# Performance work log

Measured on AMD Instinct MI355X. Metric: run time of the kernel, lower is better.

Reference implementation:

```python
import jax, jax.numpy as jnp
import numpy as np

B, T, D, H = 8, 256, 1024, 512
NUM_SPANS = T * (T + 1) // 2          # triangular span enumeration
K = int(2.0 * T)                      # pruning_ratio * num_tokens
NUM_GOLD = 10
NEG = -1e20                           # allennlp replace_masked_values fill

# static triangular (start, end) index tables: for start in range(T): for end in range(start, T)
_starts = np.repeat(np.arange(T), np.arange(T, 0, -1))
_ends = np.concatenate([np.arange(s, T) for s in range(T)])
START_IDX = jnp.asarray(_starts, dtype=jnp.int32)
END_IDX = jnp.asarray(_ends, dtype=jnp.int32)


def setup_inputs() -> dict:
    key = jax.random.key(0)
    ks = jax.random.split(key, 8)
    inputs = jax.random.normal(ks[0], (B, T, D), dtype=jnp.float32)
    input_mask = jnp.ones((B, T), dtype=jnp.int32)
    # gold spans with start <= end, all in range (sorted along last dim)
    answer_spans = jnp.sort(jax.random.randint(ks[1], (B, NUM_GOLD, 2), 0, T), axis=-1)
    sD = 1.0 / np.sqrt(D)
    sH = 1.0 / np.sqrt(H)
    W_start = jax.random.uniform(ks[2], (D, H), jnp.float32, -sD, sD)
    b_start = jax.random.uniform(ks[3], (H,), jnp.float32, -sD, sD)
    W_end = jax.random.uniform(ks[4], (D, H), jnp.float32, -sD, sD)
    b_end = jax.random.uniform(ks[5], (H,), jnp.float32, -sD, sD)
    w_score = jax.random.uniform(ks[6], (H, 1), jnp.float32, -sH, sH)
    b_score = jax.random.uniform(ks[7], (1,), jnp.float32, -sH, sH)
    return {"inputs": inputs, "input_mask": input_mask, "answer_spans": answer_spans,
            "W_start": W_start, "b_start": b_start, "W_end": W_end, "b_end": b_end,
            "w_score": w_score, "b_score": b_score}


def reference(inputs, input_mask, answer_spans, W_start, b_start, W_end, b_end, w_score, b_score):
    # SpanRepAssembly: project starts/ends, pairwise-sum over triangular spans
    hs = inputs @ W_start + b_start                        # [B,T,H]
    he = inputs @ W_end + b_end                            # [B,T,H]
    span_hidden = hs[:, START_IDX, :] + he[:, END_IDX, :]  # [B,S,H]
    m = input_mask.astype(bool)
    span_mask = m[:, START_IDX] & m[:, END_IDX]            # [B,S]

    # span scorer: ReLU -> Linear(H,1)
    scores = jax.nn.relu(span_hidden) @ w_score + b_score  # [B,S,1]
    scores = jnp.where(span_mask[..., None], scores, NEG)

    # Pruner: top-k by score, indices sorted ascending, gather
    _, top_idx = jax.lax.top_k(scores[..., 0], K)          # [B,K]
    top_idx = jnp.sort(top_idx, axis=1)
    top_logits = jnp.take_along_axis(scores, top_idx[..., None], axis=1)       # [B,K,1]
    top_mask = jnp.take_along_axis(span_mask, top_idx, axis=1)[..., None].astype(jnp.float32)
    top_probs = jax.nn.sigmoid(top_logits) * top_mask

    # gold prediction map (union policy): labels[b, tri_index(span)] = 1
    s0 = answer_spans[..., 0].astype(jnp.int32)
    e0 = answer_spans[..., 1].astype(jnp.int32)
    gmask = (s0 >= 0)
    arg_idx = (2 * s0 * T - s0 * s0 + s0) // 2 + (e0 - s0)
    arg_idx = jnp.where(gmask, arg_idx, 0)
    labels = jnp.zeros((B, NUM_SPANS), jnp.float32)
    labels = labels.at[jnp.arange(B)[:, None], arg_idx].max(gmask.astype(jnp.float32))
    pred = jnp.take_along_axis(labels[..., None], top_idx[..., None], axis=1)  # [B,K,1]

    # BCE-with-logits, weight=top_mask, reduction='sum' (stable form)
    l = top_logits
    bce = jnp.maximum(l, 0.0) - l * pred + jnp.log1p(jnp.exp(-jnp.abs(l)))
    loss = jnp.sum(top_mask * bce)
    return top_probs, loss
```

## Files before the change

### kernel.cpp

```cpp
#include <hip/hip_runtime.h>
#include <hip/hip_bf16.h>
#include <math.h>

#define BB 8
#define TT 256
#define DD 1024
#define HH 512
#define NSPANS 32896
#define KK 512
#define NEGV -1e20f
#define NCH 32
#define CHSZ 1028
#define NT16 72

typedef __attribute__((ext_vector_type(8))) short bf16x8;
typedef __attribute__((ext_vector_type(4))) float f32x4;

__device__ inline unsigned short f2bf(float f) {
    unsigned u = __float_as_uint(f);
    return (unsigned short)((u + 0x7FFFu + ((u >> 16) & 1u)) >> 16);
}
__device__ inline float bf2f(unsigned short u) {
    return __uint_as_float(((unsigned)u) << 16);
}
__device__ inline void split3(float v, unsigned short& a, unsigned short& b,
                              unsigned short& c) {
    a = f2bf(v);           float r  = v - bf2f(a);
    b = f2bf(r);           float r2 = r - bf2f(b);
    c = f2bf(r2);
}

__global__ __launch_bounds__(256) void prep(
    const float* __restrict__ X,
    const float* __restrict__ Ws, const float* __restrict__ We,
    unsigned short* __restrict__ x0, unsigned short* __restrict__ x1,
    unsigned short* __restrict__ x2, unsigned short* __restrict__ wt,
    unsigned* __restrict__ zp)
{
    const int blk = blockIdx.x;
    const int tid = threadIdx.x;

    if (blk < 2048) {
        const int i4 = blk * 256 + tid;
        const float4 v = ((const float4*)X)[i4];
        const float vv[4] = {v.x, v.y, v.z, v.w};
        ushort4 h0, h1, h2;
        unsigned short* p0 = (unsigned short*)&h0;
        unsigned short* p1 = (unsigned short*)&h1;
        unsigned short* p2 = (unsigned short*)&h2;
        #pragma unroll
        for (int j = 0; j < 4; ++j) split3(vv[j], p0[j], p1[j], p2[j]);
        ((ushort4*)x0)[i4] = h0;
        ((ushort4*)x1)[i4] = h1;
        ((ushort4*)x2)[i4] = h2;
    } else if (blk < 3072) {
        __shared__ float lt[32][33];
        const int blk2 = blk - 2048;
        const int z   = blk2 >> 9;
        const int rem = blk2 & 511;
        const int k0  = (rem >> 4) * 32;
        const int h0  = (rem & 15) * 32;

        const float* Wz = z ? We : Ws;
        {
            const int row = tid >> 3, c4 = tid & 7;
            const float4 v = *(const float4*)&Wz[(k0 + row) * HH + h0 + c4 * 4];
            lt[row][c4*4 + 0] = v.x;
            lt[row][c4*4 + 1] = v.y;
            lt[row][c4*4 + 2] = v.z;
            lt[row][c4*4 + 3] = v.w;
        }
        __syncthreads();
        {
            const int n = h0 + (tid >> 3), kq = tid & 7;
            ushort4 o0, o1, o2;
            unsigned short* q0 = (unsigned short*)&o0;
            unsigned short* q1 = (unsigned short*)&o1;
            unsigned short* q2 = (unsigned short*)&o2;
            #pragma unroll
            for (int u = 0; u < 4; ++u)
                split3(lt[kq*4 + u][tid >> 3], q0[u], q1[u], q2[u]);
            unsigned short* base = wt + (size_t)z * 3 * 524288;
            const int off = n * 1024 + k0 + kq * 4;
            *(ushort4*)&base[0 * 524288 + off] = o0;
            *(ushort4*)&base[1 * 524288 + off] = o1;
            *(ushort4*)&base[2 * 524288 + off] = o2;
        }
    } else {
        const int i = (blk - 3072) * 256 + tid;
        for (int k = i; k < 32777; k += 32 * 256) zp[k] = 0u;
    }
}

__global__ __launch_bounds__(256) void gemm_mfma(
    const unsigned short* __restrict__ xs,
    const unsigned short* __restrict__ wt,
    const float* __restrict__ bs, const float* __restrict__ be,
    float* __restrict__ hs, float* __restrict__ he)
{
    const int bid = blockIdx.x;
    const int lg  = ((bid & 7) << 6) + (bid >> 3);
    const int z   = lg >> 8;
    const int my  = (lg & 255) >> 3, nx = lg & 7;
    const int m0 = my * 64, n0 = nx * 64;

    const unsigned short* __restrict__ W = wt + (size_t)z * 3 * 524288;
    const float* __restrict__ bias = z ? be : bs;
    float* __restrict__ Y = z ? he : hs;

    __shared__ __align__(16) unsigned short la[3][64][40];
    __shared__ __align__(16) unsigned short lb[3][64][40];

    const int tid = threadIdx.x;
    const int wave = tid >> 6, lane = tid & 63;
    const int wm = (wave >> 1) * 32, wn = (wave & 1) * 32;
    const int rA = lane & 15, kq = lane >> 4;

    f32x4 acc[2][2];
    #pragma unroll
    for (int i = 0; i < 2; ++i)
        #pragma unroll
        for (int j = 0; j < 2; ++j) acc[i][j] = (f32x4){0.f, 0.f, 0.f, 0.f};

    const int lrow = tid >> 2, lc4 = tid & 3;

    for (int kt = 0; kt < 32; ++kt) {
        const int k0 = kt * 32;
        __syncthreads();
        #pragma unroll
        for (int sp = 0; sp < 3; ++sp) {
            *(int4*)&la[sp][lrow][lc4 * 8] =
                *(const int4*)&xs[(size_t)sp * 2097152 + (m0 + lrow) * 1024 + k0 + lc4 * 8];
            *(int4*)&lb[sp][lrow][lc4 * 8] =
                *(const int4*)&W[(size_t)sp * 524288 + (n0 + lrow) * 1024 + k0 + lc4 * 8];
        }
        __syncthreads();

        bf16x8 af[3][2], bg[3][2];
        #pragma unroll
        for (int sp = 0; sp < 3; ++sp) {
            #pragma unroll
            for (int f = 0; f < 2; ++f) {
                af[sp][f] = *(const bf16x8*)&la[sp][wm + f * 16 + rA][kq * 8];
                bg[sp][f] = *(const bf16x8*)&lb[sp][wn + f * 16 + rA][kq * 8];
            }
        }
        #pragma unroll
        for (int fm = 0; fm < 2; ++fm)
            #pragma unroll
            for (int fn = 0; fn < 2; ++fn) {
                acc[fm][fn] = __builtin_amdgcn_mfma_f32_16x16x32_bf16(
                    af[0][fm], bg[0][fn], acc[fm][fn], 0, 0, 0);
                acc[fm][fn] = __builtin_amdgcn_mfma_f32_16x16x32_bf16(
                    af[0][fm], bg[1][fn], acc[fm][fn], 0, 0, 0);
                acc[fm][fn] = __builtin_amdgcn_mfma_f32_16x16x32_bf16(
                    af[1][fm], bg[0][fn], acc[fm][fn], 0, 0, 0);
                acc[fm][fn] = __builtin_amdgcn_mfma_f32_16x16x32_bf16(
                    af[1][fm], bg[1][fn], acc[fm][fn], 0, 0, 0);
                acc[fm][fn] = __builtin_amdgcn_mfma_f32_16x16x32_bf16(
                    af[0][fm], bg[2][fn], acc[fm][fn], 0, 0, 0);
                acc[fm][fn] = __builtin_amdgcn_mfma_f32_16x16x32_bf16(
                    af[2][fm], bg[0][fn], acc[fm][fn], 0, 0, 0);
            }
    }

    const int col = lane & 15, rq = lane >> 4;
    #pragma unroll
    for (int fm = 0; fm < 2; ++fm)
        #pragma unroll
        for (int fn = 0; fn < 2; ++fn) {
            const int nn = n0 + wn + fn * 16 + col;
            const float bv = bias[nn];
            #pragma unroll
            for (int r = 0; r < 4; ++r) {
                const int mm = m0 + wm + fm * 16 + rq * 4 + r;
                Y[mm * HH + nn] = acc[fm][fn][r] + bv;
            }
        }
}

__device__ inline unsigned f2key(float f) {
    unsigned u = __float_as_uint(f);
    return u ^ ((u & 0x80000000u) ? 0xFFFFFFFFu : 0x80000000u);
}

__global__ __launch_bounds__(128) void span_scores(
    const float* __restrict__ hs, const float* __restrict__ he,
    const float* __restrict__ w_score, const float* __restrict__ b_score,
    const int* __restrict__ input_mask, float* __restrict__ scores,
    unsigned* __restrict__ hist12)
{
    const int bx = blockIdx.x;
    const int b = bx / NT16;
    int tI = bx - b * NT16;
    int i = 0, cnt = 8;
    while (tI >= cnt) { tI -= cnt; ++i; cnt = 8 - (i >> 1); }
    const int j = (i >> 1) + tI;
    const int s0 = i * 16, e0 = j * 32;

    __shared__ __align__(16) float shs[16][132];
    __shared__ __align__(16) float she[32][132];
    __shared__ __align__(16) float swc[128];
    __shared__ unsigned lh[2048];

    const int tid = threadIdx.x;
    const float4* hs4 = (const float4*)hs;
    const float4* he4 = (const float4*)he;

    for (int idx = tid; idx < 2048; idx += 128) lh[idx] = 0;

    const int ii = tid >> 4, jj = tid & 15;

    float4 acc[2][2];
    #pragma unroll
    for (int p = 0; p < 2; ++p)
        #pragma unroll
        for (int q = 0; q < 2; ++q) acc[p][q] = make_float4(0.f, 0.f, 0.f, 0.f);

    for (int ck = 0; ck < 4; ++ck) {
        const int kc = ck * 128;
        __syncthreads();
        #pragma unroll
        for (int l = 0; l < 12; ++l) {
            const int idx = l * 128 + tid;
            const int row = idx >> 5, c4 = idx & 31;
            if (row < 16) {
                *(float4*)&shs[row][c4 * 4] =
                    hs4[((b*TT + s0 + row) * HH + kc) / 4 + c4];
            } else {
                *(float4*)&she[row - 16][c4 * 4] =
                    he4[((b*TT + e0 + row - 16) * HH + kc) / 4 + c4];
            }
        }
        if (tid < 32) *(float4*)&swc[tid * 4] =
            ((const float4*)w_score)[kc / 4 + tid];
        __syncthreads();

        #pragma unroll 4
        for (int c4 = 0; c4 < 32; ++c4) {
            const float4 w  = *(const float4*)&swc[c4 * 4];
            const float4 a0 = *(const float4*)&shs[ii][c4 * 4];
            const float4 a1 = *(const float4*)&shs[ii + 8][c4 * 4];
            const float4 v0 = *(const float4*)&she[jj][c4 * 4];
            const float4 v1 = *(const float4*)&she[jj + 16][c4 * 4];
            #pragma unroll
            for (int p = 0; p < 2; ++p) {
                const float4 a = p ? a1 : a0;
                #pragma unroll
                for (int q = 0; q < 2; ++q) {
                    const float4 v = q ? v1 : v0;
                    acc[p][q].x += fmaxf(a.x + v.x, 0.f) * w.x;
                    acc[p][q].y += fmaxf(a.y + v.y, 0.f) * w.y;
                    acc[p][q].z += fmaxf(a.z + v.z, 0.f) * w.z;
                    acc[p][q].w += fmaxf(a.w + v.w, 0.f) * w.w;
                }
            }
        }
    }

    const float bsc = b_score[0];
    #pragma unroll
    for (int p = 0; p < 2; ++p) {
        const int s = s0 + ii + p * 8;
        #pragma unroll
        for (int q = 0; q < 2; ++q) {
            const int e = e0 + jj + q * 16;
            if (e >= s) {
                const float4 a4 = acc[p][q];
                float scv = (a4.x + a4.y) + (a4.z + a4.w) + bsc;
                if (!(input_mask[b*TT + s] && input_mask[b*TT + e])) scv = NEGV;
                scores[b*NSPANS + s*TT - (s*(s-1))/2 + (e - s)] = scv;
                const unsigned bin = f2key(scv) >> 20;
                atomicAdd(&lh[bin >> 1], 1u << ((bin & 1u) * 16));
            }
        }
    }
    __syncthreads();

    for (int idx = tid; idx < 2048; idx += 128) {
        const unsigned w = lh[idx];
        const unsigned lo = w & 0xFFFFu, hi = w >> 16;
        if (lo) atomicAdd(&hist12[b*4096 + 2*idx],     lo);
        if (hi) atomicAdd(&hist12[b*4096 + 2*idx + 1], hi);
    }
}

__global__ __launch_bounds__(256) void findcompact(
    const float* __restrict__ scores, const unsigned* __restrict__ hist12,
    unsigned* __restrict__ thrInfo,
    unsigned* __restrict__ cand, unsigned* __restrict__ candCnt)
{
    const int b = blockIdx.x >> 5, ch = blockIdx.x & 31;
    const unsigned* h = hist12 + b * 4096;
    const int tid = threadIdx.x;
    const int lane = tid & 63, wave = tid >> 6;

    const int topbin = 4095 - tid * 16;
    unsigned psum = 0;
    #pragma unroll
    for (int j = 0; j < 16; ++j) psum += h[topbin - j];

    unsigned inc = psum;
    #pragma unroll
    for (int off = 1; off < 64; off <<= 1) {
        unsigned v = __shfl_up(inc, off);
        if (lane >= off) inc += v;
    }
    __shared__ unsigned wsum4[4], wpre4[4];
    __shared__ unsigned shp[2];
    if (lane == 63) wsum4[wave] = inc;
    __syncthreads();
    if (tid == 0) { unsigned c = 0; for (int w = 0; w < 4; ++w) { wpre4[w] = c; c += wsum4[w]; } }
    __syncthreads();

    const unsigned before = wpre4[wave] + inc - psum;
    if (before < KK && before + psum >= KK) {
        unsigned cum = before;
        int bin = topbin;
        #pragma unroll
        for (int j = 0; j < 16; ++j) {
            const unsigned c = h[topbin - j];
            if (cum + c >= KK) { bin = topbin - j; break; }
            cum += c;
        }
        shp[0] = (unsigned)bin;
        shp[1] = KK - cum;
        thrInfo[b*4 + 0] = (unsigned)bin;
        thrInfo[b*4 + 1] = KK - cum;
    }
    __syncthreads();
    const unsigned p12 = shp[0];

    const float* sc = scores + b * NSPANS;
    const int base = ch * CHSZ;
    for (int i = base + tid; i < base + CHSZ; i += 256) {
        const unsigned key = f2key(sc[i]);
        if ((key >> 20) == p12) {
            const unsigned pos = atomicAdd(&candCnt[b], 1u);
            cand[b*NSPANS + pos] = key & 0xFFFFFu;
        }
    }
}

__global__ __launch_bounds__(1024) void refine(
    const unsigned* __restrict__ cand, const unsigned* __restrict__ candCnt,
    const float* __restrict__ scores,
    unsigned* __restrict__ thrInfo, unsigned* __restrict__ chunkBase)
{
    const int b = blockIdx.x;
    const unsigned* cd = cand + b*NSPANS;
    const unsigned n = candCnt[b];
    const unsigned remaining = thrInfo[b*4 + 1];
    const int tid = threadIdx.x;
    const int lane = tid & 63, wave = tid >> 6;

    __shared__ unsigned hist[1024];
    __shared__ unsigned wsum[16], wpre[16];
    __shared__ unsigned sh[2], shT[2];

    hist[tid] = 0;
    __syncthreads();
    for (unsigned i = tid; i < n; i += 1024) atomicAdd(&hist[(cd[i] >> 10) & 1023u], 1u);
    __syncthreads();
    {
        const unsigned psum = hist[1023 - tid];
        unsigned inc = psum;
        #pragma unroll
        for (int off = 1; off < 64; off <<= 1) {
            unsigned v = __shfl_up(inc, off);
            if (lane >= off) inc += v;
        }
        if (lane == 63) wsum[wave] = inc;
        __syncthreads();
        if (tid == 0) { unsigned c = 0; for (int w = 0; w < 16; ++w) { wpre[w] = c; c += wsum[w]; } }
        __syncthreads();
        const unsigned before = wpre[wave] + inc - psum;
        if (before < remaining && before + psum >= remaining && psum > 0) {
            sh[0] = 1023u - (unsigned)tid;
            sh[1] = remaining - before;
        }
        __syncthreads();
    }
    const unsigned b1 = sh[0], rem1 = sh[1];
    __syncthreads();

    hist[tid] = 0;
    __syncthreads();
    for (unsigned i = tid; i < n; i += 1024) {
        const unsigned v = cd[i];
        if (((v >> 10) & 1023u) == b1) atomicAdd(&hist[v & 1023u], 1u);
    }
    __syncthreads();
    {
        const unsigned psum = hist[1023 - tid];
        unsigned inc = psum;
        #pragma unroll
        for (int off = 1; off < 64; off <<= 1) {
            unsigned v = __shfl_up(inc, off);
            if (lane >= off) inc += v;
        }
        if (lane == 63) wsum[wave] = inc;
        __syncthreads();
        if (tid == 0) { unsigned c = 0; for (int w = 0; w < 16; ++w) { wpre[w] = c; c += wsum[w]; } }
        __syncthreads();
        const unsigned before = wpre[wave] + inc - psum;
        if (before < rem1 && before + psum >= rem1 && psum > 0) {
            const unsigned thrv = (thrInfo[b*4 + 0] << 20) | (b1 << 10) | (1023u - (unsigned)tid);
            thrInfo[b*4 + 2] = thrv;
            thrInfo[b*4 + 3] = rem1 - before;
            shT[0] = thrv;
            shT[1] = rem1 - before;
        }
    }
    __syncthreads();
    const unsigned thr = shT[0], ties = shT[1];

    __shared__ unsigned cg[NCH], ce[NCH];
    const float* sc = scores + b*NSPANS;
    #pragma unroll
    for (int q = 0; q < 2; ++q) {
        const int ch = wave*2 + q;
        const int base = ch*CHSZ, end = base + CHSZ;
        unsigned g = 0, e = 0;
        for (int i = base + lane; i < end; i += 64) {
            const unsigned key = f2key(sc[i]);
            g += (key > thr); e += (key == thr);
        }
        #pragma unroll
        for (int off = 32; off; off >>= 1) { g += __shfl_down(g, off); e += __shfl_down(e, off); }
        if (lane == 0) { cg[ch] = g; ce[ch] = e; }
    }
    __syncthreads();

    if (tid == 0) {
        unsigned out = 0, eqp = 0;
        for (int c = 0; c < NCH; ++c) {
            chunkBase[(b*NCH + c)*2 + 0] = out;
            chunkBase[(b*NCH + c)*2 + 1] = eqp;
            const unsigned room = (eqp >= ties) ? 0u : (ties - eqp);
            const unsigned taken = (ce[c] < room) ? ce[c] : room;
            out += cg[c] + taken;
            eqp += ce[c];
        }
    }
}

__global__ __launch_bounds__(256) void scatter_final(
    const float* __restrict__ scores, const unsigned* __restrict__ thrInfo,
    const unsigned* __restrict__ chunkBase, const int* __restrict__ answer_spans,
    float* __restrict__ chunkLoss, unsigned* __restrict__ ticket,
    float* __restrict__ out)
{
    const int b = blockIdx.x >> 5, ch = blockIdx.x & 31;
    const float* sc = scores + b*NSPANS;
    const unsigned thr = thrInfo[b*4 + 2], ties = thrInfo[b*4 + 3];
    unsigned outPos = chunkBase[(b*NCH + ch)*2 + 0];
    unsigned eqPos  = chunkBase[(b*NCH + ch)*2 + 1];

    const int tid = threadIdx.x, wave = tid >> 6, lane = tid & 63;
    const unsigned long long lmask = (1ull << lane) - 1ull;
    __shared__ unsigned wS[4], wE[4];
    __shared__ int gold[10];
    __shared__ float wLoss[4];
    __shared__ unsigned lastFlag;

    if (tid < 10) {
        const int s0 = answer_spans[b*20 + tid*2];
        const int e0 = answer_spans[b*20 + tid*2 + 1];
        gold[tid] = (s0 >= 0) ? ((2*s0*TT - s0*s0 + s0)/2 + (e0 - s0)) : -1;
    }
    __syncthreads();

    float lsum = 0.f;
    const int base = ch*CHSZ;
    for (int seg = base; seg < base + CHSZ; seg += 256) {
        const int i = seg + tid;
        const bool valid = (i < base + CHSZ);
        const float v = valid ? sc[i] : 0.f;
        const unsigned key = valid ? f2key(v) : 0u;
        const bool g  = valid && key > thr;
        const bool eq = valid && key == thr;

        const unsigned long long meq = __ballot(eq);
        if (lane == 0) wE[wave] = (unsigned)__popcll(meq);
        __syncthreads();

        unsigned eqPre = eqPos;
        for (int w = 0; w < wave; ++w) eqPre += wE[w];
        const unsigned myEqRank = eqPre + (unsigned)__popcll(meq & lmask);
        const bool sel = g || (eq && myEqRank < ties);

        const unsigned long long msel = __ballot(sel);
        if (lane == 0) wS[wave] = (unsigned)__popcll(msel);
        __syncthreads();

        unsigned selPre = outPos;
        for (int w = 0; w < wave; ++w) selPre += wS[w];
        if (sel) {
            const unsigned pos = b*KK + selPre + (unsigned)__popcll(msel & lmask);
            float prob = 0.f;
            if (v > -1e19f) {
                prob = 1.f / (1.f + expf(-v));
                float pred = 0.f;
                #pragma unroll
                for (int gq = 0; gq < 10; ++gq)
                    if (gold[gq] == i) pred = 1.f;
                lsum += fmaxf(v, 0.f) - v*pred + log1pf(expf(-fabsf(v)));
            }
            out[pos] = prob;
        }

        unsigned totS = 0, totE = 0;
        #pragma unroll
        for (int w = 0; w < 4; ++w) { totS += wS[w]; totE += wE[w]; }
        __syncthreads();
        outPos += totS; eqPos += totE;
    }

    #pragma unroll
    for (int off = 32; off; off >>= 1) lsum += __shfl_down(lsum, off);
    if (lane == 0) wLoss[wave] = lsum;
    __syncthreads();
    if (tid == 0) {
        chunkLoss[b*NCH + ch] = (wLoss[0] + wLoss[1]) + (wLoss[2] + wLoss[3]);
        __threadfence();
        lastFlag = atomicAdd(ticket, 1u);
    }
    __syncthreads();

    if (lastFlag == BB*NCH - 1) {
        __threadfence();
        float cl = atomicAdd(&chunkLoss[tid], 0.f);
        #pragma unroll
        for (int off = 32; off; off >>= 1) cl += __shfl_down(cl, off);
        if (lane == 0) wLoss[wave] = cl;
        __syncthreads();
        if (tid == 0)
            out[BB*KK] = (wLoss[0] + wLoss[1]) + (wLoss[2] + wLoss[3]);
    }
}

extern "C" void kernel_launch(void* const* d_in, const int* in_sizes, int n_in,
                              void* d_out, int out_size, void* d_ws, size_t ws_size,
                              hipStream_t stream)
{
    const float* inputs       = (const float*)d_in[0];
    const int*   input_mask   = (const int*)  d_in[1];
    const int*   answer_spans = (const int*)  d_in[2];
    const float* W_start      = (const float*)d_in[3];
    const float* b_start      = (const float*)d_in[4];
    const float* W_end        = (const float*)d_in[5];
    const float* b_end        = (const float*)d_in[6];
    const float* w_score      = (const float*)d_in[7];
    const float* b_score      = (const float*)d_in[8];
    float* out = (float*)d_out;
    unsigned* ws = (unsigned*)d_ws;

    float*    hs       = (float*)(ws);
    float*    he       = (float*)(ws + 1048576);
    float*    scores   = (float*)(ws + 2097152);
    unsigned* thrInfo  = ws + 2364416;
    unsigned* chunkBase= ws + 2364448;
    unsigned* hist12   = ws + 2364960;
    unsigned* candCnt  = ws + 2397728;
    unsigned* ticket   = ws + 2397736;
    unsigned short* xs = (unsigned short*)(ws + 2397740);
    unsigned short* wt = (unsigned short*)(ws + 5543468);
    float*    chunkLoss= (float*)(ws + 8689196);
    unsigned* cand     = (unsigned*)hs;

    prep<<<3104, 256, 0, stream>>>(inputs, W_start, W_end,
                                   xs, xs + 2097152, xs + 4194304, wt, hist12);

    gemm_mfma<<<512, 256, 0, stream>>>(xs, wt, b_start, b_end, hs, he);

    span_scores<<<BB*NT16, 128, 0, stream>>>(hs, he, w_score, b_score, input_mask,
                                             scores, hist12);

    findcompact  <<<BB*NCH, 256, 0, stream>>>(scores, hist12, thrInfo, cand, candCnt);
    refine       <<<BB, 1024, 0, stream>>>(cand, candCnt, scores, thrInfo, chunkBase);
    scatter_final<<<BB*NCH, 256, 0, stream>>>(scores, thrInfo, chunkBase,
                                              answer_spans, chunkLoss, ticket, out);
}
```

Before: 128.1 us.

## Split K across two wave groups per GEMM block, reducing partial sums through LDS

Each GEMM block now runs 512 threads: two groups of four waves, each covering half of the K dimension with its own LDS tiles. Group 1 writes its partial accumulators to shared memory and group 0 adds them, plus the bias, before storing the output. The aim is more waves in flight per output tile, to hide load latency in the MFMA main loop. The cost is double the LDS footprint, an extra barrier and reduction step, and heavier per-block register and LDS use that may lower how many blocks fit per CU. The workspace offset of chunkLoss is also moved to directly follow the weight buffer.

After: 127.9 us. No clear change (-0.2%).

```diff
diff --git a/kernel.cpp b/kernel.cpp
--- a/kernel.cpp
+++ b/kernel.cpp
@@ -92,7 +92,7 @@
     }
 }
 
-__global__ __launch_bounds__(256) void gemm_mfma(
+__global__ __launch_bounds__(512) void gemm_mfma(
     const unsigned short* __restrict__ xs,
     const unsigned short* __restrict__ wt,
     const float* __restrict__ bs, const float* __restrict__ be,
@@ -108,13 +108,18 @@
     const float* __restrict__ bias = z ? be : bs;
     float* __restrict__ Y = z ? he : hs;
 
-    __shared__ __align__(16) unsigned short la[3][64][40];
-    __shared__ __align__(16) unsigned short lb[3][64][40];
+    __shared__ __align__(16) unsigned short la[2][3][64][40];
+    __shared__ __align__(16) unsigned short lb[2][3][64][40];
 
     const int tid = threadIdx.x;
-    const int wave = tid >> 6, lane = tid & 63;
-    const int wm = (wave >> 1) * 32, wn = (wave & 1) * 32;
+    const int wave8 = tid >> 6;
+    const int grp = wave8 >> 2;
+    const int wavein = wave8 & 3;
+    const int lane = tid & 63;
+    const int t = tid & 255;
+    const int wm = (wavein >> 1) * 32, wn = (wavein & 1) * 32;
     const int rA = lane & 15, kq = lane >> 4;
+    const int kb = grp * 512;
 
     f32x4 acc[2][2];
     #pragma unroll
@@ -122,16 +127,16 @@
         #pragma unroll
         for (int j = 0; j < 2; ++j) acc[i][j] = (f32x4){0.f, 0.f, 0.f, 0.f};
 
-    const int lrow = tid >> 2, lc4 = tid & 3;
-
-    for (int kt = 0; kt < 32; ++kt) {
-        const int k0 = kt * 32;
+    const int lrow = t >> 2, lc4 = t & 3;
+
+    for (int kt = 0; kt < 16; ++kt) {
+        const int k0 = kb + kt * 32;
         __syncthreads();
         #pragma unroll
         for (int sp = 0; sp < 3; ++sp) {
-            *(int4*)&la[sp][lrow][lc4 * 8] =
+            *(int4*)&la[grp][sp][lrow][lc4 * 8] =
                 *(const int4*)&xs[(size_t)sp * 2097152 + (m0 + lrow) * 1024 + k0 + lc4 * 8];
-            *(int4*)&lb[sp][lrow][lc4 * 8] =
+            *(int4*)&lb[grp][sp][lrow][lc4 * 8] =
                 *(const int4*)&W[(size_t)sp * 524288 + (n0 + lrow) * 1024 + k0 + lc4 * 8];
         }
         __syncthreads();
@@ -141,8 +146,8 @@
         for (int sp = 0; sp < 3; ++sp) {
             #pragma unroll
             for (int f = 0; f < 2; ++f) {
-                af[sp][f] = *(const bf16x8*)&la[sp][wm + f * 16 + rA][kq * 8];
-                bg[sp][f] = *(const bf16x8*)&lb[sp][wn + f * 16 + rA][kq * 8];
+                af[sp][f] = *(const bf16x8*)&la[grp][sp][wm + f * 16 + rA][kq * 8];
+                bg[sp][f] = *(const bf16x8*)&lb[grp][sp][wn + f * 16 + rA][kq * 8];
             }
         }
         #pragma unroll
@@ -164,19 +169,32 @@
             }
     }
 
-    const int col = lane & 15, rq = lane >> 4;
-    #pragma unroll
-    for (int fm = 0; fm < 2; ++fm)
-        #pragma unroll
-        for (int fn = 0; fn < 2; ++fn) {
-            const int nn = n0 + wn + fn * 16 + col;
-            const float bv = bias[nn];
+    __syncthreads();
+    float* red = (float*)&la[0][0][0][0];
+    if (grp == 1) {
+        #pragma unroll
+        for (int fm = 0; fm < 2; ++fm)
             #pragma unroll
-            for (int r = 0; r < 4; ++r) {
-                const int mm = m0 + wm + fm * 16 + rq * 4 + r;
-                Y[mm * HH + nn] = acc[fm][fn][r] + bv;
+            for (int fn = 0; fn < 2; ++fn)
+                *(f32x4*)&red[t * 16 + (fm * 2 + fn) * 4] = acc[fm][fn];
+    }
+    __syncthreads();
+    if (grp == 0) {
+        const int col = lane & 15, rq = lane >> 4;
+        #pragma unroll
+        for (int fm = 0; fm < 2; ++fm)
+            #pragma unroll
+            for (int fn = 0; fn < 2; ++fn) {
+                const int nn = n0 + wn + fn * 16 + col;
+                const float bv = bias[nn];
+                const f32x4 r4 = *(const f32x4*)&red[t * 16 + (fm * 2 + fn) * 4];
+                #pragma unroll
+                for (int r = 0; r < 4; ++r) {
+                    const int mm = m0 + wm + fm * 16 + rq * 4 + r;
+                    Y[mm * HH + nn] = acc[fm][fn][r] + r4[r] + bv;
+                }
             }
-        }
+    }
 }
 
 __device__ inline unsigned f2key(float f) {
@@ -566,13 +584,13 @@
     unsigned* ticket   = ws + 2397736;
     unsigned short* xs = (unsigned short*)(ws + 2397740);
     unsigned short* wt = (unsigned short*)(ws + 5543468);
-    float*    chunkLoss= (float*)(ws + 8689196);
+    float*    chunkLoss= (float*)(ws + 7116332);
     unsigned* cand     = (unsigned*)hs;
 
     prep<<<3104, 256, 0, stream>>>(inputs, W_start, W_end,
                                    xs, xs + 2097152, xs + 4194304, wt, hist12);
 
-    gemm_mfma<<<512, 256, 0, stream>>>(xs, wt, b_start, b_end, hs, he);
+    gemm_mfma<<<512, 512, 0, stream>>>(xs, wt, b_start, b_end, hs, he);
 
     span_scores<<<BB*NT16, 128, 0, stream>>>(hs, he, w_score, b_score, input_mask,
                                              scores, hist12);
```
